# Optimization experiments

Hardware: AMD Instinct MI355X
Metric: run time of the kernel (lower is better)

## Reference

```python
import jax, jax.numpy as jnp
import numpy as np

B, S, E, H = 2, 2048, 1024, 16
D = E // H  # head_dim = 64


def setup_inputs() -> dict:
    key = jax.random.key(0)
    ks = jax.random.split(key, 5)
    return {
        "hidden_states": jax.random.normal(ks[0], (B, S, E), jnp.float32),
        "c_attn_w": jax.random.normal(ks[1], (E, 3 * E), jnp.float32) * 0.02,
        "c_attn_b": jax.random.normal(ks[2], (3 * E,), jnp.float32) * 0.02,
        "c_proj_w": jax.random.normal(ks[3], (E, E), jnp.float32) * 0.02,
        "c_proj_b": jax.random.normal(ks[4], (E,), jnp.float32) * 0.02,
    }


def reference(hidden_states, c_attn_w, c_attn_b, c_proj_w, c_proj_b):
    # Conv1D: y = x @ W + b, W is [in, out]
    qkv = hidden_states @ c_attn_w + c_attn_b            # [B,S,3E]
    q, k, v = jnp.split(qkv, 3, axis=-1)                 # each [B,S,E]

    def split_heads(t):
        return t.reshape(B, S, H, D).transpose(0, 2, 1, 3)  # [B,H,S,D]

    q, k, v = split_heads(q), split_heads(k), split_heads(v)

    # scores scaled by 1/sqrt(head_dim) (scale_attn_weights=True)
    scores = jnp.einsum("bhqd,bhkd->bhqk", q, k) / jnp.asarray(
        np.sqrt(D), dtype=q.dtype
    )
    # causal mask: torch.where(causal, scores, finfo.min)
    causal = jnp.tril(jnp.ones((S, S), dtype=bool))
    mask_value = jnp.finfo(scores.dtype).min
    scores = jnp.where(causal[None, None], scores, mask_value)

    attn = jax.nn.softmax(scores, axis=-1)               # [B,H,S,S]
    out = jnp.einsum("bhqk,bhkd->bhqd", attn, v)          # [B,H,S,D]
    out = out.transpose(0, 2, 1, 3).reshape(B, S, E)      # merge heads
    out = out @ c_proj_w + c_proj_b                       # c_proj
    return out
```

## Files before the change

kernel.cpp:

```cpp
#include <hip/hip_runtime.h>
#include <stdint.h>

#define LOG2E 1.4426950408889634f
#define QSCALE (0.125f * LOG2E)

using u16 = unsigned short;
using u32 = unsigned int;

typedef __attribute__((ext_vector_type(8))) short short8;
typedef __attribute__((ext_vector_type(4))) float f32x4;
typedef __attribute__((ext_vector_type(16))) float f32x16;

__device__ __forceinline__ u16 f32_bf16(float f) {
  union { float f; u32 u; } v; v.f = f;
  u32 u = v.u;
  u += 0x7FFF + ((u >> 16) & 1);
  return (u16)(u >> 16);
}

__device__ __forceinline__ float max3f(float a, float b, float c) {
  return fmaxf(fmaxf(a, b), c);
}

__device__ __forceinline__ void gload_lds16(const void* g, void* l) {
  __builtin_amdgcn_global_load_lds(
      (const __attribute__((address_space(1))) u32*)(uintptr_t)g,
      (__attribute__((address_space(3))) u32*)(u32)(uintptr_t)l, 16, 0, 0);
}


__global__ __launch_bounds__(256) void cvt_f32_bf16(const float* __restrict__ in,
                                                    u16* __restrict__ out, int n4) {
  for (int i = blockIdx.x * blockDim.x + threadIdx.x; i < n4;
       i += gridDim.x * blockDim.x) {
    float4 v = ((const float4*)in)[i];
    union { u16 h[4]; uint2 u; } o;
    o.h[0] = f32_bf16(v.x); o.h[1] = f32_bf16(v.y);
    o.h[2] = f32_bf16(v.z); o.h[3] = f32_bf16(v.w);
    ((uint2*)out)[i] = o.u;
  }
}

__global__ __launch_bounds__(256) void transpose_bf16(const float* __restrict__ in,
                                                      u16* __restrict__ out,
                                                      int K, int N) {
  __shared__ float t[32][33];
  const int n0 = blockIdx.x * 32, k0 = blockIdx.y * 32;
  const int tx = threadIdx.x, ty = threadIdx.y;
#pragma unroll
  for (int j = 0; j < 32; j += 8)
    t[ty + j][tx] = in[(size_t)(k0 + ty + j) * N + n0 + tx];
  __syncthreads();
#pragma unroll
  for (int j = 0; j < 32; j += 8)
    out[(size_t)(n0 + ty + j) * K + k0 + tx] = f32_bf16(t[tx][ty + j]);
}

template <int MODE>
__global__ __launch_bounds__(256) void gemm_bt(
    const u16* __restrict__ A, const u16* __restrict__ Bt,
    const float* __restrict__ bias,
    u16* __restrict__ qb, u16* __restrict__ kb, u16* __restrict__ vtb,
    float* __restrict__ fout) {
  __shared__ u16 lA[128 * 32];
  __shared__ u16 lB[128 * 32];
  const int tid = threadIdx.x;
  const int w = tid >> 6, l = tid & 63;
  const int bm = blockIdx.y, bn = blockIdx.x;
  const size_t m0 = (size_t)bm * 128, n0 = (size_t)bn * 128;
  const int wr = w >> 1, wc = w & 1;

  f32x4 acc[4][4] = {};

  const int arow = w * 16 + (l >> 2);
  const int acol = (l & 3) * 8;
  const u16* gA = A + (m0 + arow) * 1024 + acol;
  const u16* gB = Bt + (n0 + arow) * 1024 + acol;
  u16* lAw = lA + w * 512;
  u16* lBw = lB + w * 512;

  for (int k0 = 0; k0 < 1024; k0 += 32) {
    gload_lds16(gA + k0, lAw);
    gload_lds16(gA + k0 + 64 * 1024, lAw + 2048);
    gload_lds16(gB + k0, lBw);
    gload_lds16(gB + k0 + 64 * 1024, lBw + 2048);
    __syncthreads();
    short8 af[4], bf[4];
#pragma unroll
    for (int m = 0; m < 4; ++m)
      af[m] = *(const short8*)&lA[(wr * 64 + m * 16 + (l & 15)) * 32 + (l >> 4) * 8];
#pragma unroll
    for (int n = 0; n < 4; ++n)
      bf[n] = *(const short8*)&lB[(wc * 64 + n * 16 + (l & 15)) * 32 + (l >> 4) * 8];
#pragma unroll
    for (int m = 0; m < 4; ++m)
#pragma unroll
      for (int n = 0; n < 4; ++n)
        acc[m][n] = __builtin_amdgcn_mfma_f32_16x16x32_bf16(af[m], bf[n], acc[m][n], 0, 0, 0);
    __syncthreads();
  }

  if (MODE == 0) {
#pragma unroll
    for (int m = 0; m < 4; ++m) {
      const int row = (int)m0 + wr * 64 + m * 16 + ((l >> 4) << 2);
      const int b = row >> 11, s = row & 2047;
#pragma unroll
      for (int n = 0; n < 4; ++n) {
        const int col = (int)n0 + wc * 64 + n * 16 + (l & 15);
        const int part = col >> 10;
        const int h = (col & 1023) >> 6, d = col & 63;
        const float bv = bias[col];
        const size_t bh = (size_t)(b * 16 + h);
#pragma unroll
        for (int r = 0; r < 4; ++r) {
          const float v = acc[m][n][r] + bv;
          const int ss = s + r;
          if (part == 0)
            qb[(bh * 2048 + ss) * 64 + d] = f32_bf16(v * QSCALE);
          else if (part == 1)
            kb[(bh * 2048 + ss) * 64 + d] = f32_bf16(v);
          else
            vtb[(bh * 64 + d) * 2048 + ss] = f32_bf16(v);
        }
      }
    }
  } else {
#pragma unroll
    for (int m = 0; m < 4; ++m) {
      const size_t row = m0 + wr * 64 + m * 16 + ((l >> 4) << 2);
#pragma unroll
      for (int n = 0; n < 4; ++n) {
        const size_t col = n0 + wc * 64 + n * 16 + (l & 15);
        const float bv = bias[col];
#pragma unroll
        for (int r = 0; r < 4; ++r)
          fout[(row + r) * 1024 + col] = acc[m][n][r] + bv;
      }
    }
  }
}

__global__ __launch_bounds__(256) void attn_fwd6(const u16* __restrict__ Qb,
                                                 const u16* __restrict__ Kb,
                                                 const u16* __restrict__ Vt,
                                                 u16* __restrict__ AO) {
  __shared__ u16 lK[2][4096];
  __shared__ u16 lV[2][4096];
  const int tid = threadIdx.x;
  const int l = tid & 63, w = tid >> 6;
  const int lq = l & 31, hi = l >> 5;
  const int bid = blockIdx.x;
  const int xcd = bid & 7, idx = bid >> 3;
  const int bh = xcd * 4 + (idx & 3);
  const int qb = 15 - (idx >> 2);
  const int qw = qb * 128 + w * 32;
  const int q = qw + lq;
  const int cdiag = 2 * qb + (w >> 1);
  const int NT = 2 * qb + 2;

  const u16* Qh = Qb + (size_t)bh * 131072;
  const u16* Kh = Kb + (size_t)bh * 131072;
  const u16* Vh = Vt + (size_t)bh * 131072;

  short8 qf[4];
#pragma unroll
  for (int kk = 0; kk < 4; ++kk)
    qf[kk] = *(const short8*)&Qh[(size_t)q * 64 + kk * 16 + hi * 8];

  f32x16 oA = {}, oB = {};
  float m = -3.0e38f, lsum = 0.f;

  const int srow = l >> 3, sslot = l & 7;
  const int swz = ((sslot ^ srow) << 3);
  const u16* kbase = Kh + (16 * w + srow) * 64 + swz;
  const u16* vbase = Vh + (size_t)(16 * w + srow) * 2048 + swz;
  char* lKw0 = (char*)&lK[0][0] + 2 * w * 1024;
  char* lVw0 = (char*)&lV[0][0] + 2 * w * 1024;

  auto stage = [&](int buf, int c) {
    const u16* ks = kbase + c * 4096;
    const u16* vs = vbase + c * 64;
    char* kd = lKw0 + buf * 8192;
    char* vd = lVw0 + buf * 8192;
    gload_lds16(ks, kd);
    gload_lds16(ks + 512, kd + 1024);
    gload_lds16(vs, vd);
    gload_lds16(vs + 16384, vd + 1024);
  };

  const int swsl = (lq & 7);

  auto pack16 = [&](const f32x16& st, short8& lo, short8& hi8) {
    u32 pk[8];
#pragma unroll
    for (int t2 = 0; t2 < 8; ++t2)
      asm("v_cvt_pk_bf16_f32 %0, %1, %2" : "=v"(pk[t2]) : "v"(st[2 * t2]), "v"(st[2 * t2 + 1]));
    u32 a0 = pk[0], a1 = pk[2]; asm("v_permlane32_swap_b32 %0, %1" : "+v"(a0), "+v"(a1));
    u32 a2 = pk[1], a3 = pk[3]; asm("v_permlane32_swap_b32 %0, %1" : "+v"(a2), "+v"(a3));
    u32 c0 = pk[4], c1 = pk[6]; asm("v_permlane32_swap_b32 %0, %1" : "+v"(c0), "+v"(c1));
    u32 c2 = pk[5], c3 = pk[7]; asm("v_permlane32_swap_b32 %0, %1" : "+v"(c2), "+v"(c3));
    union { u32 u[4]; short8 s; } f0, f1;
    f0.u[0] = a0; f0.u[1] = a2; f0.u[2] = a1; f0.u[3] = a3;
    f1.u[0] = c0; f1.u[1] = c2; f1.u[2] = c1; f1.u[3] = c3;
    lo = f0.s; hi8 = f1.s;
  };

  auto body64 = [&](int buf, bool mask2) {
    const char* kb = (const char*)&lK[buf][0] + lq * 128;
    const char* vb = (const char*)&lV[buf][0] + lq * 128;
    short8 kf0[4], kf1[4];
#pragma unroll
    for (int kk = 0; kk < 4; ++kk) {
      const int sl = ((2 * kk + hi) ^ swsl) << 4;
      kf0[kk] = *(const short8*)(kb + sl);
      kf1[kk] = *(const short8*)(kb + 4096 + sl);
    }
    f32x16 st0 = {}, st1 = {};
    __builtin_amdgcn_s_setprio(1);
#pragma unroll
    for (int kk = 0; kk < 4; ++kk)
      st0 = __builtin_amdgcn_mfma_f32_32x32x16_bf16(kf0[kk], qf[kk], st0, 0, 0, 0);
#pragma unroll
    for (int kk = 0; kk < 4; ++kk)
      st1 = __builtin_amdgcn_mfma_f32_32x32x16_bf16(kf1[kk], qf[kk], st1, 0, 0, 0);
    __builtin_amdgcn_s_setprio(0);

    short8 vfA[4], vfB[4];
#pragma unroll
    for (int ks = 0; ks < 4; ++ks) {
      const int sl = ((2 * ks + hi) ^ swsl) << 4;
      vfA[ks] = *(const short8*)(vb + sl);
      vfB[ks] = *(const short8*)(vb + 4096 + sl);
    }

    if (mask2) {
      const int qm = lq - hi * 4;
#pragma unroll
      for (int r = 0; r < 16; ++r) {
        const int t = (r & 3) + 8 * (r >> 2);
        if (t > qm) st1[r] = -3.0e38f;
      }
    }

    float a0 = max3f(st0[0], st0[1], st0[2]);
    float a1 = max3f(st0[3], st0[4], st0[5]);
    float a2 = max3f(st0[6], st0[7], st0[8]);
    float a3 = max3f(st0[9], st0[10], st0[11]);
    float a4 = max3f(st0[12], st0[13], st0[14]);
    float a5 = max3f(st0[15], st1[0], st1[1]);
    float a6 = max3f(st1[2], st1[3], st1[4]);
    float a7 = max3f(st1[5], st1[6], st1[7]);
    float a8 = max3f(st1[8], st1[9], st1[10]);
    float a9 = max3f(st1[11], st1[12], st1[13]);
    float a10 = fmaxf(st1[14], st1[15]);
    float b0 = max3f(a0, a1, a2);
    float b1 = max3f(a3, a4, a5);
    float b2 = max3f(a6, a7, a8);
    float b3 = max3f(a9, a10, b0);
    float pm = max3f(b1, b2, b3);
    pm = fmaxf(pm, __shfl_xor(pm, 32));

    if (!__all(pm <= m + 8.0f)) {
      const float mn = fmaxf(m, pm);
      const float alpha = __builtin_amdgcn_exp2f(m - mn);
      lsum *= alpha;
#pragma unroll
      for (int r = 0; r < 16; ++r) { oA[r] *= alpha; oB[r] *= alpha; }
      m = mn;
    }

#pragma unroll
    for (int r = 0; r < 16; ++r) st0[r] = __builtin_amdgcn_exp2f(st0[r] - m);
#pragma unroll
    for (int r = 0; r < 16; ++r) st1[r] = __builtin_amdgcn_exp2f(st1[r] - m);

    float s0 = (st0[0] + st0[1]) + (st0[2] + st0[3]);
    float s1 = (st0[4] + st0[5]) + (st0[6] + st0[7]);
    float s2 = (st0[8] + st0[9]) + (st0[10] + st0[11]);
    float s3 = (st0[12] + st0[13]) + (st0[14] + st0[15]);
    float s4 = (st1[0] + st1[1]) + (st1[2] + st1[3]);
    float s5 = (st1[4] + st1[5]) + (st1[6] + st1[7]);
    float s6 = (st1[8] + st1[9]) + (st1[10] + st1[11]);
    float s7 = (st1[12] + st1[13]) + (st1[14] + st1[15]);
    float rs = ((s0 + s1) + (s2 + s3)) + ((s4 + s5) + (s6 + s7));
    rs += __shfl_xor(rs, 32);
    lsum += rs;

    short8 pf0, pf1, pf2, pf3;
    pack16(st0, pf0, pf1);
    pack16(st1, pf2, pf3);

    __builtin_amdgcn_s_setprio(1);
    oA = __builtin_amdgcn_mfma_f32_32x32x16_bf16(vfA[0], pf0, oA, 0, 0, 0);
    oA = __builtin_amdgcn_mfma_f32_32x32x16_bf16(vfA[1], pf1, oA, 0, 0, 0);
    oA = __builtin_amdgcn_mfma_f32_32x32x16_bf16(vfA[2], pf2, oA, 0, 0, 0);
    oA = __builtin_amdgcn_mfma_f32_32x32x16_bf16(vfA[3], pf3, oA, 0, 0, 0);
    oB = __builtin_amdgcn_mfma_f32_32x32x16_bf16(vfB[0], pf0, oB, 0, 0, 0);
    oB = __builtin_amdgcn_mfma_f32_32x32x16_bf16(vfB[1], pf1, oB, 0, 0, 0);
    oB = __builtin_amdgcn_mfma_f32_32x32x16_bf16(vfB[2], pf2, oB, 0, 0, 0);
    oB = __builtin_amdgcn_mfma_f32_32x32x16_bf16(vfB[3], pf3, oB, 0, 0, 0);
    __builtin_amdgcn_s_setprio(0);
  };

  auto body32m = [&](int buf) {
    const char* kb = (const char*)&lK[buf][0] + lq * 128;
    const char* vb = (const char*)&lV[buf][0] + lq * 128;
    short8 kf0[4];
#pragma unroll
    for (int kk = 0; kk < 4; ++kk)
      kf0[kk] = *(const short8*)(kb + (((2 * kk + hi) ^ swsl) << 4));
    f32x16 st0 = {};
    __builtin_amdgcn_s_setprio(1);
#pragma unroll
    for (int kk = 0; kk < 4; ++kk)
      st0 = __builtin_amdgcn_mfma_f32_32x32x16_bf16(kf0[kk], qf[kk], st0, 0, 0, 0);
    __builtin_amdgcn_s_setprio(0);

    short8 vfA[2], vfB[2];
#pragma unroll
    for (int ks = 0; ks < 2; ++ks) {
      const int sl = ((2 * ks + hi) ^ swsl) << 4;
      vfA[ks] = *(const short8*)(vb + sl);
      vfB[ks] = *(const short8*)(vb + 4096 + sl);
    }

    const int qm = lq - hi * 4;
#pragma unroll
    for (int r = 0; r < 16; ++r) {
      const int t = (r & 3) + 8 * (r >> 2);
      if (t > qm) st0[r] = -3.0e38f;
    }
    float a0 = max3f(st0[0], st0[1], st0[2]);
    float a1 = max3f(st0[3], st0[4], st0[5]);
    float a2 = max3f(st0[6], st0[7], st0[8]);
    float a3 = max3f(st0[9], st0[10], st0[11]);
    float a4 = max3f(st0[12], st0[13], st0[14]);
    float b0 = max3f(a0, a1, a2);
    float b1 = max3f(a3, a4, st0[15]);
    float pm = fmaxf(b0, b1);
    pm = fmaxf(pm, __shfl_xor(pm, 32));
    if (!__all(pm <= m + 8.0f)) {
      const float mn = fmaxf(m, pm);
      const float alpha = __builtin_amdgcn_exp2f(m - mn);
      lsum *= alpha;
#pragma unroll
      for (int r = 0; r < 16; ++r) { oA[r] *= alpha; oB[r] *= alpha; }
      m = mn;
    }
#pragma unroll
    for (int r = 0; r < 16; ++r) st0[r] = __builtin_amdgcn_exp2f(st0[r] - m);
    float s0 = (st0[0] + st0[1]) + (st0[2] + st0[3]);
    float s1 = (st0[4] + st0[5]) + (st0[6] + st0[7]);
    float s2 = (st0[8] + st0[9]) + (st0[10] + st0[11]);
    float s3 = (st0[12] + st0[13]) + (st0[14] + st0[15]);
    float rs = (s0 + s1) + (s2 + s3);
    rs += __shfl_xor(rs, 32);
    lsum += rs;

    short8 pf0, pf1;
    pack16(st0, pf0, pf1);
    __builtin_amdgcn_s_setprio(1);
    oA = __builtin_amdgcn_mfma_f32_32x32x16_bf16(vfA[0], pf0, oA, 0, 0, 0);
    oA = __builtin_amdgcn_mfma_f32_32x32x16_bf16(vfA[1], pf1, oA, 0, 0, 0);
    oB = __builtin_amdgcn_mfma_f32_32x32x16_bf16(vfB[0], pf0, oB, 0, 0, 0);
    oB = __builtin_amdgcn_mfma_f32_32x32x16_bf16(vfB[1], pf1, oB, 0, 0, 0);
    __builtin_amdgcn_s_setprio(0);
  };

  stage(0, 0);
  __syncthreads();
  int cur = 0;
  for (int c = 0; c < NT; ++c) {
    if (c + 1 < NT) stage(cur ^ 1, c + 1);
    if (c < cdiag) body64(cur, false);
    else if (c == cdiag) { if (w & 1) body64(cur, true); else body32m(cur); }
    __syncthreads();
    cur ^= 1;
  }

  const float rl = __builtin_amdgcn_rcpf(lsum);
  const int b = bh >> 4, h = bh & 15;
  u16* orow = AO + ((size_t)(b * 2048 + q)) * 1024 + h * 64;
#pragma unroll
  for (int g = 0; g < 4; ++g) {
    float e0 = oA[4 * g] * rl, e1 = oA[4 * g + 1] * rl;
    float e2 = oA[4 * g + 2] * rl, e3 = oA[4 * g + 3] * rl;
    float f0 = oB[4 * g] * rl, f1 = oB[4 * g + 1] * rl;
    float f2 = oB[4 * g + 2] * rl, f3 = oB[4 * g + 3] * rl;
    u32 w0, w1, w2, w3;
    asm("v_cvt_pk_bf16_f32 %0, %1, %2" : "=v"(w0) : "v"(e0), "v"(e1));
    asm("v_cvt_pk_bf16_f32 %0, %1, %2" : "=v"(w1) : "v"(e2), "v"(e3));
    asm("v_cvt_pk_bf16_f32 %0, %1, %2" : "=v"(w2) : "v"(f0), "v"(f1));
    asm("v_cvt_pk_bf16_f32 %0, %1, %2" : "=v"(w3) : "v"(f2), "v"(f3));
    uint2 uA; uA.x = w0; uA.y = w1;
    uint2 uB; uB.x = w2; uB.y = w3;
    *(uint2*)&orow[8 * g + 4 * hi] = uA;
    *(uint2*)&orow[32 + 8 * g + 4 * hi] = uB;
  }
}


extern "C" void kernel_launch(void* const* d_in, const int* in_sizes, int n_in,
                              void* d_out, int out_size, void* d_ws, size_t ws_size,
                              hipStream_t stream) {
  const float* hs = (const float*)d_in[0];
  const float* w1 = (const float*)d_in[1];
  const float* b1 = (const float*)d_in[2];
  const float* w2 = (const float*)d_in[3];
  const float* b2 = (const float*)d_in[4];
  float* out = (float*)d_out;

  char* ws = (char*)d_ws;
  u16* Xb  = (u16*)(ws);
  u16* W1t = (u16*)(ws + (8ull  << 20));
  u16* W2t = (u16*)(ws + (14ull << 20));
  u16* Qb  = (u16*)(ws + (16ull << 20));
  u16* Kb  = (u16*)(ws + (24ull << 20));
  u16* Vtb = (u16*)(ws + (32ull << 20));
  u16* AO  = (u16*)(ws + (40ull << 20));

  cvt_f32_bf16<<<dim3(2048), dim3(256), 0, stream>>>(hs, Xb, 4096 * 1024 / 4);
  transpose_bf16<<<dim3(96, 32), dim3(32, 8), 0, stream>>>(w1, W1t, 1024, 3072);
  transpose_bf16<<<dim3(32, 32), dim3(32, 8), 0, stream>>>(w2, W2t, 1024, 1024);
  gemm_bt<0><<<dim3(24, 32), dim3(256), 0, stream>>>(Xb, W1t, b1, Qb, Kb, Vtb, nullptr);
  attn_fwd6<<<dim3(512), dim3(256), 0, stream>>>(Qb, Kb, Vtb, AO);
  gemm_bt<1><<<dim3(8, 32), dim3(256), 0, stream>>>(AO, W2t, b2, nullptr, nullptr, nullptr, out);
}
```

Before: 125.1 us.

## Use triple-buffered swizzled GEMM and smaller attention blocks with transposed V epilogue

Replaces the GEMM with a three-slot LDS ring that prefetches two K-tiles ahead, uses XOR-swizzled LDS layout, and relies on vmcnt waits with a single barrier per iteration instead of two syncthreads. For the V part of the QKV GEMM it swaps MFMA operands so the transposed V store writes contiguous sequence positions. Attention is retiled to 64-query blocks of 128 threads with 1024 blocks, each wave staging more K/V rows. The goal is to overlap loads with MFMA, cut barrier stalls and LDS bank conflicts, and improve attention load balance, at the cost of more LDS per GEMM block and a more complex causal-diagonal split.

```diff
diff --git a/kernel.cpp b/kernel.cpp
--- a/kernel.cpp
+++ b/kernel.cpp
@@ -57,91 +57,144 @@
 }
 
 template <int MODE>
-__global__ __launch_bounds__(256) void gemm_bt(
+__global__ __launch_bounds__(256) void gemm_ring3(
     const u16* __restrict__ A, const u16* __restrict__ Bt,
     const float* __restrict__ bias,
     u16* __restrict__ qb, u16* __restrict__ kb, u16* __restrict__ vtb,
     float* __restrict__ fout) {
-  __shared__ u16 lA[128 * 32];
-  __shared__ u16 lB[128 * 32];
+  __shared__ u16 lds[3 * 8192];
   const int tid = threadIdx.x;
-  const int w = tid >> 6, l = tid & 63;
+  const int l = tid & 63, w = tid >> 6;
+  const int l15 = l & 15, l4 = l >> 4;
+  const int wr = w >> 1, wc = w & 1;
   const int bm = blockIdx.y, bn = blockIdx.x;
-  const size_t m0 = (size_t)bm * 128, n0 = (size_t)bn * 128;
-  const int wr = w >> 1, wc = w & 1;
+  const size_t m0 = (size_t)bm * 128;
+  const int nb = bn * 128;
+  const bool sw = (MODE == 0) && (bn >= 16);
+
+  const u16* gsrc[4];
+#pragma unroll
+  for (int q = 0; q < 4; ++q) {
+    const int c = q * 256 + tid;
+    const int mat = c >> 9, pc = c & 511;
+    const int pair = pc >> 3, s8 = pc & 7;
+    const int us8 = s8 ^ (pair & 7);
+    const int grow = 2 * pair + (us8 >> 2), kslot = us8 & 3;
+    gsrc[q] = (mat ? Bt + (size_t)(nb + grow) * 1024
+                   : A + (m0 + grow) * 1024) + kslot * 8;
+  }
+
+  auto stage = [&](int slot, int t) {
+#pragma unroll
+    for (int q = 0; q < 4; ++q)
+      gload_lds16(gsrc[q] + t * 32,
+                  (char*)lds + slot * 16384 + q * 4096 + w * 1024);
+  };
+
+  auto rdA = [&](int slot, int mI) -> short8 {
+    const int row = wr * 64 + mI * 16 + l15;
+    const int pair = row >> 1;
+    const int s8 = (((row & 1) << 2) + l4) ^ (pair & 7);
+    return *(const short8*)((const char*)lds + slot * 16384 + pair * 128 + s8 * 16);
+  };
+  auto rdB = [&](int slot, int nI) -> short8 {
+    const int row = wc * 64 + nI * 16 + l15;
+    const int pair = row >> 1;
+    const int s8 = (((row & 1) << 2) + l4) ^ (pair & 7);
+    return *(const short8*)((const char*)lds + slot * 16384 + 8192 + pair * 128 + s8 * 16);
+  };
 
   f32x4 acc[4][4] = {};
 
-  const int arow = w * 16 + (l >> 2);
-  const int acol = (l & 3) * 8;
-  const u16* gA = A + (m0 + arow) * 1024 + acol;
-  const u16* gB = Bt + (n0 + arow) * 1024 + acol;
-  u16* lAw = lA + w * 512;
-  u16* lBw = lB + w * 512;
-
-  for (int k0 = 0; k0 < 1024; k0 += 32) {
-    gload_lds16(gA + k0, lAw);
-    gload_lds16(gA + k0 + 64 * 1024, lAw + 2048);
-    gload_lds16(gB + k0, lBw);
-    gload_lds16(gB + k0 + 64 * 1024, lBw + 2048);
-    __syncthreads();
+  stage(0, 0);
+  stage(1, 1);
+
+  int slot = 0;
+  for (int t = 0; t < 32; ++t) {
+    if (t == 31) asm volatile("s_waitcnt vmcnt(0)" ::: "memory");
+    else         asm volatile("s_waitcnt vmcnt(4)" ::: "memory");
+    __builtin_amdgcn_s_barrier();
+    __builtin_amdgcn_sched_barrier(0);
     short8 af[4], bf[4];
 #pragma unroll
-    for (int m = 0; m < 4; ++m)
-      af[m] = *(const short8*)&lA[(wr * 64 + m * 16 + (l & 15)) * 32 + (l >> 4) * 8];
-#pragma unroll
-    for (int n = 0; n < 4; ++n)
-      bf[n] = *(const short8*)&lB[(wc * 64 + n * 16 + (l & 15)) * 32 + (l >> 4) * 8];
-#pragma unroll
-    for (int m = 0; m < 4; ++m)
+    for (int n = 0; n < 4; ++n) bf[n] = rdB(slot, n);
+#pragma unroll
+    for (int mI = 0; mI < 4; ++mI) af[mI] = rdA(slot, mI);
+    if (t + 2 < 32) {
+      int ss = slot + 2; if (ss >= 3) ss -= 3;
+      stage(ss, t + 2);
+    }
+    if (!sw) {
 #pragma unroll
       for (int n = 0; n < 4; ++n)
-        acc[m][n] = __builtin_amdgcn_mfma_f32_16x16x32_bf16(af[m], bf[n], acc[m][n], 0, 0, 0);
-    __syncthreads();
-  }
-
-  if (MODE == 0) {
-#pragma unroll
-    for (int m = 0; m < 4; ++m) {
-      const int row = (int)m0 + wr * 64 + m * 16 + ((l >> 4) << 2);
+#pragma unroll
+        for (int mI = 0; mI < 4; ++mI)
+          acc[mI][n] = __builtin_amdgcn_mfma_f32_16x16x32_bf16(af[mI], bf[n], acc[mI][n], 0, 0, 0);
+    } else {
+#pragma unroll
+      for (int n = 0; n < 4; ++n)
+#pragma unroll
+        for (int mI = 0; mI < 4; ++mI)
+          acc[mI][n] = __builtin_amdgcn_mfma_f32_16x16x32_bf16(bf[n], af[mI], acc[mI][n], 0, 0, 0);
+    }
+    ++slot; if (slot == 3) slot = 0;
+  }
+
+  if (MODE == 1) {
+#pragma unroll
+    for (int mI = 0; mI < 4; ++mI) {
+      const size_t row = m0 + wr * 64 + mI * 16 + (l4 << 2);
+#pragma unroll
+      for (int n = 0; n < 4; ++n) {
+        const size_t col = (size_t)nb + wc * 64 + n * 16 + l15;
+        const float bv = bias[col];
+#pragma unroll
+        for (int r = 0; r < 4; ++r)
+          fout[(row + r) * 1024 + col] = acc[mI][n][r] + bv;
+      }
+    }
+  } else if (!sw) {
+#pragma unroll
+    for (int mI = 0; mI < 4; ++mI) {
+      const int row = (int)m0 + wr * 64 + mI * 16 + (l4 << 2);
       const int b = row >> 11, s = row & 2047;
 #pragma unroll
       for (int n = 0; n < 4; ++n) {
-        const int col = (int)n0 + wc * 64 + n * 16 + (l & 15);
+        const int col = nb + wc * 64 + n * 16 + l15;
         const int part = col >> 10;
         const int h = (col & 1023) >> 6, d = col & 63;
         const float bv = bias[col];
         const size_t bh = (size_t)(b * 16 + h);
+        u16* dst = (part == 0) ? qb : kb;
+        const float sc = (part == 0) ? QSCALE : 1.0f;
+#pragma unroll
+        for (int r = 0; r < 4; ++r)
+          dst[(bh * 2048 + (s + r)) * 64 + d] = f32_bf16((acc[mI][n][r] + bv) * sc);
+      }
+    }
+  } else {
+#pragma unroll
+    for (int mI = 0; mI < 4; ++mI) {
+      const int scol = (int)m0 + wr * 64 + mI * 16 + l15;
+      const int b = scol >> 11, s = scol & 2047;
+#pragma unroll
+      for (int n = 0; n < 4; ++n) {
+        const int colg = nb + wc * 64 + n * 16 + (l4 << 2);
+        const float4 bv4 = *(const float4*)&bias[colg];
+        const float bvr[4] = { bv4.x, bv4.y, bv4.z, bv4.w };
 #pragma unroll
         for (int r = 0; r < 4; ++r) {
-          const float v = acc[m][n][r] + bv;
-          const int ss = s + r;
-          if (part == 0)
-            qb[(bh * 2048 + ss) * 64 + d] = f32_bf16(v * QSCALE);
-          else if (part == 1)
-            kb[(bh * 2048 + ss) * 64 + d] = f32_bf16(v);
-          else
-            vtb[(bh * 64 + d) * 2048 + ss] = f32_bf16(v);
+          const int dcol = colg + r - 2048;
+          const int h = dcol >> 6, d = dcol & 63;
+          const size_t bh = (size_t)(b * 16 + h);
+          vtb[bh * 131072 + (size_t)d * 2048 + s] = f32_bf16(acc[mI][n][r] + bvr[r]);
         }
       }
     }
-  } else {
-#pragma unroll
-    for (int m = 0; m < 4; ++m) {
-      const size_t row = m0 + wr * 64 + m * 16 + ((l >> 4) << 2);
-#pragma unroll
-      for (int n = 0; n < 4; ++n) {
-        const size_t col = n0 + wc * 64 + n * 16 + (l & 15);
-        const float bv = bias[col];
-#pragma unroll
-        for (int r = 0; r < 4; ++r)
-          fout[(row + r) * 1024 + col] = acc[m][n][r] + bv;
-      }
-    }
-  }
-}
-
-__global__ __launch_bounds__(256) void attn_fwd6(const u16* __restrict__ Qb,
+  }
+}
+
+__global__ __launch_bounds__(128) void attn_fwd7(const u16* __restrict__ Qb,
                                                  const u16* __restrict__ Kb,
                                                  const u16* __restrict__ Vt,
                                                  u16* __restrict__ AO) {
@@ -153,11 +206,9 @@
   const int bid = blockIdx.x;
   const int xcd = bid & 7, idx = bid >> 3;
   const int bh = xcd * 4 + (idx & 3);
-  const int qb = 15 - (idx >> 2);
-  const int qw = qb * 128 + w * 32;
-  const int q = qw + lq;
-  const int cdiag = 2 * qb + (w >> 1);
-  const int NT = 2 * qb + 2;
+  const int qb = 31 - (idx >> 2);
+  const int q = qb * 64 + w * 32 + lq;
+  const int NT = qb + 1;
 
   const u16* Qh = Qb + (size_t)bh * 131072;
   const u16* Kh = Kb + (size_t)bh * 131072;
@@ -173,20 +224,19 @@
 
   const int srow = l >> 3, sslot = l & 7;
   const int swz = ((sslot ^ srow) << 3);
-  const u16* kbase = Kh + (16 * w + srow) * 64 + swz;
-  const u16* vbase = Vh + (size_t)(16 * w + srow) * 2048 + swz;
-  char* lKw0 = (char*)&lK[0][0] + 2 * w * 1024;
-  char* lVw0 = (char*)&lV[0][0] + 2 * w * 1024;
+  const u16* kbase = Kh + (32 * w + srow) * 64 + swz;
+  const u16* vbase = Vh + (size_t)(32 * w + srow) * 2048 + swz;
 
   auto stage = [&](int buf, int c) {
     const u16* ks = kbase + c * 4096;
     const u16* vs = vbase + c * 64;
-    char* kd = lKw0 + buf * 8192;
-    char* vd = lVw0 + buf * 8192;
-    gload_lds16(ks, kd);
-    gload_lds16(ks + 512, kd + 1024);
-    gload_lds16(vs, vd);
-    gload_lds16(vs + 16384, vd + 1024);
+    char* kd = (char*)&lK[buf][0] + w * 4096;
+    char* vd = (char*)&lV[buf][0] + w * 4096;
+#pragma unroll
+    for (int i = 0; i < 4; ++i) {
+      gload_lds16(ks + 512 * i, kd + 1024 * i);
+      gload_lds16(vs + 16384 * i, vd + 1024 * i);
+    }
   };
 
   const int swsl = (lq & 7);
@@ -373,8 +423,8 @@
   int cur = 0;
   for (int c = 0; c < NT; ++c) {
     if (c + 1 < NT) stage(cur ^ 1, c + 1);
-    if (c < cdiag) body64(cur, false);
-    else if (c == cdiag) { if (w & 1) body64(cur, true); else body32m(cur); }
+    if (c < qb) body64(cur, false);
+    else { if (w) body64(cur, true); else body32m(cur); }
     __syncthreads();
     cur ^= 1;
   }
@@ -423,7 +473,7 @@
   cvt_f32_bf16<<<dim3(2048), dim3(256), 0, stream>>>(hs, Xb, 4096 * 1024 / 4);
   transpose_bf16<<<dim3(96, 32), dim3(32, 8), 0, stream>>>(w1, W1t, 1024, 3072);
   transpose_bf16<<<dim3(32, 32), dim3(32, 8), 0, stream>>>(w2, W2t, 1024, 1024);
-  gemm_bt<0><<<dim3(24, 32), dim3(256), 0, stream>>>(Xb, W1t, b1, Qb, Kb, Vtb, nullptr);
-  attn_fwd6<<<dim3(512), dim3(256), 0, stream>>>(Qb, Kb, Vtb, AO);
-  gemm_bt<1><<<dim3(8, 32), dim3(256), 0, stream>>>(AO, W2t, b2, nullptr, nullptr, nullptr, out);
-}
+  gemm_ring3<0><<<dim3(24, 32), dim3(256), 0, stream>>>(Xb, W1t, b1, Qb, Kb, Vtb, nullptr);
+  attn_fwd7<<<dim3(1024), dim3(128), 0, stream>>>(Qb, Kb, Vtb, AO);
+  gemm_ring3<1><<<dim3(8, 32), dim3(256), 0, stream>>>(AO, W2t, b2, nullptr, nullptr, nullptr, out);
+}
```

Measured after the change: 128.1 us. 1.02x slower.
